# Optimization experiments

Hardware: AMD Instinct MI355X
Metric: run time of the kernel (lower is better)

The kernel has to match this reference:

```python
import jax, jax.numpy as jnp
import numpy as np

# ---- static config (mirrors PointRend init kwargs) ----
H, W = 512, 512          # img_size
CH, CW = 128, 128        # coarse_size
FH, FW = 256, 256        # fine_size
CF = 256                 # fine_channels
NC = 3                   # num_classes (forced by MLP's hard-coded 259/131 channel counts)
NPTS = 2048              # N points
K_OVER = 3               # k oversampling
BELTA = 0.75
NUM_OVER = K_OVER * NPTS          # 6144
STEP1 = int(NPTS * BELTA)         # 1536 uncertain points
STEP2 = NPTS - STEP1              # 512 coverage points


def _xavier(key, c_out, c_in):
    std = (2.0 / (c_in + c_out)) ** 0.5
    return jax.random.normal(key, (c_out, c_in), jnp.float32) * std


def setup_inputs() -> dict:
    key = jax.random.key(0)
    k1, k2, k3, k4, k5, k6 = jax.random.split(key, 6)
    fine_grained = jax.random.normal(k1, (2, CF, FH, FW), jnp.float32)
    coarse_pre = jax.random.normal(k2, (2, NC, CH, CW), jnp.float32)
    # torch.randperm(H*W) done inside forward in the original; passed in for determinism
    random_1d_index = jax.random.permutation(k3, H * W).astype(jnp.int32)
    w1 = _xavier(k4, 256, CF + NC)   # conv1: 1x1, in=259, out=256, no bias
    w2 = _xavier(k5, 128, 256 + 3)   # conv2: in=259, out=128
    w3 = _xavier(k6, NC, 128 + 3)    # conv3: in=131, out=num_classes
    prelu_a = jnp.array(0.25, jnp.float32)  # shared single-param PReLU
    return dict(fine_grained=fine_grained, coarse_pre=coarse_pre,
                w1=w1, w2=w2, w3=w3, prelu_a=prelu_a,
                random_1d_index=random_1d_index)


def _bilinear(x, h, w):
    # matches nn.Upsample(mode='bilinear', align_corners=False)
    return jax.image.resize(x, (x.shape[0], x.shape[1], h, w), method="bilinear")


def _prelu(x, a):
    return jnp.where(x >= 0, x, a * x)


def _mlp(feat, w1, w2, w3, a):
    # feat: [B, N, C] -> channels-first [B, C, N]; BatchNorms in MLP are unused in forward.
    x = jnp.transpose(feat, (0, 2, 1))
    tail = x[:, -3:, :]  # last 3 channels appended to each layer's input
    l1 = _prelu(jnp.einsum('bcn,oc->bon', x, w1), a)
    l2 = _prelu(jnp.einsum('bcn,oc->bon', jnp.concatenate([l1, tail], 1), w2), a)
    return jnp.einsum('bcn,oc->bon', jnp.concatenate([l2, tail], 1), w3)  # [B, NC, N]


def reference(fine_grained, coarse_pre, w1, w2, w3, prelu_a, random_1d_index):
    B = fine_grained.shape[0]
    up_coarse_o = _bilinear(coarse_pre, H, W)            # [B, NC, H, W] logits
    up_coarse_sm = jax.nn.softmax(up_coarse_o, axis=1)   # softmax over classes
    up_fine = _bilinear(fine_grained, H, W)              # [B, CF, H, W]

    h_idx = random_1d_index // W
    w_idx = random_1d_index % W
    all_index = jnp.stack([h_idx, w_idx], axis=1)        # [H*W, 2]
    cand = all_index[:NUM_OVER]                          # oversampled candidates

    # vectorized replacement of the python loop: gather probs at candidates
    over_pre = up_coarse_sm[:, :, cand[:, 0], cand[:, 1]].transpose(0, 2, 1)  # [B, NUM_OVER, NC]
    top2, _ = jax.lax.top_k(over_pre, 2)
    uncertain = 1.0 - (top2[..., 0] - top2[..., 1])      # [B, NUM_OVER]
    _, u_idx = jax.lax.top_k(uncertain, STEP1)           # [B, STEP1]
    u_pts = cand[u_idx]                                  # [B, STEP1, 2]
    cov = jnp.broadcast_to(all_index[-STEP2:][None], (B, STEP2, 2))
    pts = jnp.concatenate([u_pts, cov], axis=1)          # [B, N, 2]

    # masked_select traverses the dense mask in row-major (h,w) order -> sort linear ids
    lin = pts[..., 0] * W + pts[..., 1]                  # [B, N]
    lin_sorted = jnp.sort(lin, axis=1)
    sh, sw = lin_sorted // W, lin_sorted % W
    bidx = jnp.arange(B)[:, None]
    sel_coarse = up_coarse_o[bidx, :, sh, sw]            # [B, N, NC] (pre-softmax feats)
    sel_fine = up_fine[bidx, :, sh, sw]                  # [B, N, CF]

    # faithful to torch: flat concat of the two masked_select outputs, then reshape
    feat = jnp.concatenate([sel_fine.reshape(-1), sel_coarse.reshape(-1)]).reshape(B, NPTS, -1)

    out = _mlp(feat, w1, w2, w3, prelu_a)                # [B, NC, N]
    mask = jnp.zeros((B, H, W), jnp.int32).at[bidx, pts[..., 0], pts[..., 1]].add(1)
    return out, mask
```

## Files before the change

kernel.cpp:

```cpp
#include <hip/hip_runtime.h>
#include <hip/hip_bf16.h>

#define NPTS 2048
#define NOVER 6144
#define STEP1 1536
#define STEP2 512
#define HW_TOT 262144

__device__ __forceinline__ float prelu_f(float x, float a) { return x >= 0.0f ? x : a * x; }

__device__ __forceinline__ void coarse_coords(int h, int w, float& fy, float& fx,
                                              int& y0, int& y1, int& x0, int& x1) {
  float sy = (h + 0.5f) * 0.25f - 0.5f;
  float sx = (w + 0.5f) * 0.25f - 0.5f;
  float yf = floorf(sy), xf = floorf(sx);
  fy = sy - yf; fx = sx - xf;
  int yi = (int)yf, xi = (int)xf;
  y0 = min(127, max(0, yi)); y1 = min(127, max(0, yi + 1));
  x0 = min(127, max(0, xi)); x1 = min(127, max(0, xi + 1));
}

__device__ __forceinline__ float coarse_sample(const float* __restrict__ ch, float fy, float fx,
                                               int y0, int y1, int x0, int x1) {
  float v00 = ch[(y0 << 7) + x0];
  float v01 = ch[(y0 << 7) + x1];
  float v10 = ch[(y1 << 7) + x0];
  float v11 = ch[(y1 << 7) + x1];
  return (1.0f - fy) * ((1.0f - fx) * v00 + fx * v01) + fy * ((1.0f - fx) * v10 + fx * v11);
}

__global__ __launch_bounds__(256) void pr_fill_v4(uint4* __restrict__ p) {
  p[blockIdx.x * 256 + threadIdx.x] = make_uint4(0u, 0u, 0u, 0u);
}

__global__ __launch_bounds__(256) void pr_wprep_v4(const float* __restrict__ w1,
                                                   const float* __restrict__ w2,
                                                   float* __restrict__ wT1,
                                                   float* __restrict__ wT2) {
  int gid = blockIdx.x * 256 + threadIdx.x;
  if (gid < 259 * 256) {
    int c = gid >> 8, o = gid & 255;
    wT1[c * 256 + o] = w1[o * 259 + c];
  } else {
    int g2 = gid - 259 * 256;
    if (g2 < 259 * 128) {
      int c = g2 >> 7, o = g2 & 127;
      wT2[c * 128 + o] = w2[o * 259 + c];
    }
  }
}

__global__ __launch_bounds__(256) void pr_uncert_v4(const float* __restrict__ coarse,
                                                    const int* __restrict__ ridx,
                                                    unsigned* __restrict__ keys) {
  int gid = blockIdx.x * 256 + threadIdx.x;
  if (gid >= 2 * NOVER) return;
  int b = gid / NOVER, i = gid - b * NOVER;
  int lin = ridx[i];
  int h = lin >> 9, w = lin & 511;
  float fy, fx; int y0, y1, x0, x1;
  coarse_coords(h, w, fy, fx, y0, y1, x0, x1);
  const float* cb = coarse + (((size_t)b * 3) << 14);
  float p0 = coarse_sample(cb, fy, fx, y0, y1, x0, x1);
  float p1 = coarse_sample(cb + (1 << 14), fy, fx, y0, y1, x0, x1);
  float p2 = coarse_sample(cb + (2 << 14), fy, fx, y0, y1, x0, x1);
  float m = fmaxf(p0, fmaxf(p1, p2));
  float e0 = expf(p0 - m), e1 = expf(p1 - m), e2 = expf(p2 - m);
  float s = e0 + e1 + e2;
  float q0 = e0 / s, q1 = e1 / s, q2 = e2 / s;
  float a0 = q0, a1 = q1, a2 = q2, tmp;
  if (a0 < a1) { tmp = a0; a0 = a1; a1 = tmp; }
  if (a1 < a2) { tmp = a1; a1 = a2; a2 = tmp; }
  if (a0 < a1) { tmp = a0; a0 = a1; a1 = tmp; }
  float u = 1.0f - (a0 - a1);
  keys[gid] = __float_as_uint(u);
}

__global__ __launch_bounds__(1024) void pr_topk_v4(const unsigned* __restrict__ keys,
                                                   const int* __restrict__ ridx,
                                                   int* __restrict__ lin_sorted,
                                                   float* __restrict__ mask) {
  __shared__ unsigned kv[NOVER];
  __shared__ unsigned bitmap[8192];
  __shared__ unsigned hist[256];
  __shared__ unsigned short tiebuf[NOVER];
  __shared__ unsigned scanbuf[16];
  __shared__ unsigned selinfo[2];
  __shared__ int tiecnt;
  const int b = blockIdx.x, t = threadIdx.x;
  const int lane = t & 63, wid = t >> 6;

  for (int i = t; i < NOVER; i += 1024) kv[i] = keys[b * NOVER + i];
  for (int i = t; i < 8192; i += 1024) bitmap[i] = 0u;
  if (t == 0) { selinfo[1] = STEP1; tiecnt = 0; }
  __syncthreads();

  unsigned prefix = 0u;
  for (int pass = 0; pass < 4; ++pass) {
    const int shift = 24 - 8 * pass;
    const unsigned maskHi = (pass == 0) ? 0u : (0xFFFFFFFFu << (shift + 8));
    for (int i = t; i < 256; i += 1024) hist[i] = 0u;
    __syncthreads();
    for (int i = t; i < NOVER; i += 1024) {
      unsigned k = kv[i];
      if ((k & maskHi) == prefix) atomicAdd(&hist[(k >> shift) & 255u], 1u);
    }
    __syncthreads();
    if (t < 64) {
      unsigned h0 = hist[t * 4], h1 = hist[t * 4 + 1], h2 = hist[t * 4 + 2], h3 = hist[t * 4 + 3];
      unsigned q = h0 + h1 + h2 + h3;
      unsigned s = q;
      for (int off = 1; off < 64; off <<= 1) {
        unsigned n = __shfl_down(s, off);
        if (t + off < 64) s += n;
      }
      unsigned exq = s - q;
      unsigned R = selinfo[1];
      unsigned se3 = exq, se2 = se3 + h3, se1 = se2 + h2, se0 = se1 + h1;
      if (se3 < R && R <= se3 + h3)      { selinfo[0] = prefix | ((unsigned)(t * 4 + 3) << shift); selinfo[1] = R - se3; }
      else if (se2 < R && R <= se2 + h2) { selinfo[0] = prefix | ((unsigned)(t * 4 + 2) << shift); selinfo[1] = R - se2; }
      else if (se1 < R && R <= se1 + h1) { selinfo[0] = prefix | ((unsigned)(t * 4 + 1) << shift); selinfo[1] = R - se1; }
      else if (se0 < R && R <= se0 + h0) { selinfo[0] = prefix | ((unsigned)(t * 4 + 0) << shift); selinfo[1] = R - se0; }
    }
    __syncthreads();
    prefix = selinfo[0];
  }
  const unsigned T = prefix;
  const int r = (int)selinfo[1];

  for (int i = t; i < NOVER; i += 1024) {
    unsigned k = kv[i];
    if (k > T) {
      int lin = ridx[i];
      mask[(size_t)b * HW_TOT + lin] = 1.0f;
      atomicOr(&bitmap[lin >> 5], 1u << (lin & 31));
    } else if (k == T) {
      int pos = atomicAdd(&tiecnt, 1);
      tiebuf[pos] = (unsigned short)i;
    }
  }
  for (int i = t; i < STEP2; i += 1024) {
    int lin = ridx[HW_TOT - STEP2 + i];
    mask[(size_t)b * HW_TOT + lin] = 1.0f;
    atomicOr(&bitmap[lin >> 5], 1u << (lin & 31));
  }
  __syncthreads();
  const int m = tiecnt;
  for (int j = t; j < m; j += 1024) {
    int idx = tiebuf[j];
    int rank = 0;
    for (int jj = 0; jj < m; ++jj) rank += (tiebuf[jj] < idx) ? 1 : 0;
    if (rank < r) {
      int lin = ridx[idx];
      mask[(size_t)b * HW_TOT + lin] = 1.0f;
      atomicOr(&bitmap[lin >> 5], 1u << (lin & 31));
    }
  }
  __syncthreads();

  unsigned mySum = 0;
#pragma unroll
  for (int q = 0; q < 8; ++q) mySum += __popc(bitmap[t * 8 + q]);
  unsigned v = mySum;
  for (int off = 1; off < 64; off <<= 1) {
    unsigned n = __shfl_up(v, off);
    if (lane >= off) v += n;
  }
  if (lane == 63) scanbuf[wid] = v;
  __syncthreads();
  if (t == 0) {
    unsigned run = 0;
    for (int w16 = 0; w16 < 16; ++w16) { unsigned tmp = scanbuf[w16]; scanbuf[w16] = run; run += tmp; }
  }
  __syncthreads();
  unsigned pos = (v - mySum) + scanbuf[wid];
  for (int q = 0; q < 8; ++q) {
    unsigned word = bitmap[t * 8 + q];
    int basebit = (t * 8 + q) << 5;
    while (word) {
      int bit = __ffs(word) - 1;
      word &= word - 1;
      lin_sorted[b * NPTS + pos++] = basebit + bit;
    }
  }
}

__global__ __launch_bounds__(256) void pr_mlp_v4(const float* __restrict__ fine,
                                                 const float* __restrict__ coarse,
                                                 const float* __restrict__ wT1,
                                                 const float* __restrict__ wT2,
                                                 const float* __restrict__ w3,
                                                 const float* __restrict__ pa,
                                                 const int* __restrict__ lin_sorted,
                                                 float* __restrict__ out) {
  __shared__ __align__(16) float xs[259][16];
  __shared__ __align__(16) float l1t[256][16];
  __shared__ __align__(16) float l2t[128][16];
  const int t = threadIdx.x;
  const int g0 = blockIdx.x * 16;
  const float a = pa[0];

  for (int task = t; task < 259 * 16; task += 256) {
    int c = task >> 4, p = task & 15;
    int g = g0 + p;
    int j = g * 259 + c;
    float v;
    if (j < 1048576) {
      int nsrc = j >> 8, ch = j & 255;
      int bs = nsrc >> 11;
      int lin = lin_sorted[nsrc];
      int h = lin >> 9, w = lin & 511;
      float sy = (h + 0.5f) * 0.5f - 0.5f;
      float sx = (w + 0.5f) * 0.5f - 0.5f;
      float yf = floorf(sy), xf = floorf(sx);
      float fy = sy - yf, fx = sx - xf;
      int yi = (int)yf, xi = (int)xf;
      int y0 = min(255, max(0, yi)), y1 = min(255, max(0, yi + 1));
      int x0 = min(255, max(0, xi)), x1 = min(255, max(0, xi + 1));
      const float* base = fine + (((size_t)(bs * 256 + ch)) << 16);
      float v00 = base[(y0 << 8) + x0];
      float v01 = base[(y0 << 8) + x1];
      float v10 = base[(y1 << 8) + x0];
      float v11 = base[(y1 << 8) + x1];
      v = (1.0f - fy) * ((1.0f - fx) * v00 + fx * v01) + fy * ((1.0f - fx) * v10 + fx * v11);
    } else {
      int jj = j - 1048576;
      int nsrc = jj / 3;
      int kk = jj - nsrc * 3;
      int bs = nsrc >> 11;
      int lin = lin_sorted[nsrc];
      int h = lin >> 9, w = lin & 511;
      float fy, fx; int y0, y1, x0, x1;
      coarse_coords(h, w, fy, fx, y0, y1, x0, x1);
      v = coarse_sample(coarse + (((size_t)bs * 3 + kk) << 14), fy, fx, y0, y1, x0, x1);
    }
    xs[c][p] = v;
  }
  __syncthreads();

  {
    const int ob = (t & 63) * 4;
    const int pb = (t >> 6) * 4;
    float acc[4][4];
#pragma unroll
    for (int i = 0; i < 4; ++i)
#pragma unroll
      for (int q = 0; q < 4; ++q) acc[i][q] = 0.0f;
    for (int c = 0; c < 259; ++c) {
      const float4 wv = *(const float4*)&wT1[c * 256 + ob];
      const float4 xv = *(const float4*)&xs[c][pb];
      acc[0][0] = fmaf(wv.x, xv.x, acc[0][0]); acc[0][1] = fmaf(wv.x, xv.y, acc[0][1]);
      acc[0][2] = fmaf(wv.x, xv.z, acc[0][2]); acc[0][3] = fmaf(wv.x, xv.w, acc[0][3]);
      acc[1][0] = fmaf(wv.y, xv.x, acc[1][0]); acc[1][1] = fmaf(wv.y, xv.y, acc[1][1]);
      acc[1][2] = fmaf(wv.y, xv.z, acc[1][2]); acc[1][3] = fmaf(wv.y, xv.w, acc[1][3]);
      acc[2][0] = fmaf(wv.z, xv.x, acc[2][0]); acc[2][1] = fmaf(wv.z, xv.y, acc[2][1]);
      acc[2][2] = fmaf(wv.z, xv.z, acc[2][2]); acc[2][3] = fmaf(wv.z, xv.w, acc[2][3]);
      acc[3][0] = fmaf(wv.w, xv.x, acc[3][0]); acc[3][1] = fmaf(wv.w, xv.y, acc[3][1]);
      acc[3][2] = fmaf(wv.w, xv.z, acc[3][2]); acc[3][3] = fmaf(wv.w, xv.w, acc[3][3]);
    }
#pragma unroll
    for (int i = 0; i < 4; ++i) {
      l1t[ob + i][pb + 0] = prelu_f(acc[i][0], a);
      l1t[ob + i][pb + 1] = prelu_f(acc[i][1], a);
      l1t[ob + i][pb + 2] = prelu_f(acc[i][2], a);
      l1t[ob + i][pb + 3] = prelu_f(acc[i][3], a);
    }
  }
  __syncthreads();

  {
    const int ob = (t & 31) * 4;
    const int pb = (t >> 5) * 2;
    float acc[4][2];
#pragma unroll
    for (int i = 0; i < 4; ++i) { acc[i][0] = 0.0f; acc[i][1] = 0.0f; }
    for (int c = 0; c < 256; ++c) {
      const float4 wv = *(const float4*)&wT2[c * 128 + ob];
      const float2 xv = *(const float2*)&l1t[c][pb];
      acc[0][0] = fmaf(wv.x, xv.x, acc[0][0]); acc[0][1] = fmaf(wv.x, xv.y, acc[0][1]);
      acc[1][0] = fmaf(wv.y, xv.x, acc[1][0]); acc[1][1] = fmaf(wv.y, xv.y, acc[1][1]);
      acc[2][0] = fmaf(wv.z, xv.x, acc[2][0]); acc[2][1] = fmaf(wv.z, xv.y, acc[2][1]);
      acc[3][0] = fmaf(wv.w, xv.x, acc[3][0]); acc[3][1] = fmaf(wv.w, xv.y, acc[3][1]);
    }
#pragma unroll
    for (int kk = 0; kk < 3; ++kk) {
      const float4 wv = *(const float4*)&wT2[(256 + kk) * 128 + ob];
      const float x0 = xs[256 + kk][pb], x1 = xs[256 + kk][pb + 1];
      acc[0][0] = fmaf(wv.x, x0, acc[0][0]); acc[0][1] = fmaf(wv.x, x1, acc[0][1]);
      acc[1][0] = fmaf(wv.y, x0, acc[1][0]); acc[1][1] = fmaf(wv.y, x1, acc[1][1]);
      acc[2][0] = fmaf(wv.z, x0, acc[2][0]); acc[2][1] = fmaf(wv.z, x1, acc[2][1]);
      acc[3][0] = fmaf(wv.w, x0, acc[3][0]); acc[3][1] = fmaf(wv.w, x1, acc[3][1]);
    }
#pragma unroll
    for (int i = 0; i < 4; ++i) {
      l2t[ob + i][pb + 0] = prelu_f(acc[i][0], a);
      l2t[ob + i][pb + 1] = prelu_f(acc[i][1], a);
    }
  }
  __syncthreads();

  if (t < 48) {
    const int o3 = t % 3, p = t / 3;
    const float* wr = w3 + o3 * 131;
    float s = 0.0f;
    for (int c = 0; c < 128; ++c) s = fmaf(wr[c], l2t[c][p], s);
#pragma unroll
    for (int kk = 0; kk < 3; ++kk) s = fmaf(wr[128 + kk], xs[256 + kk][p], s);
    const int g = g0 + p;
    out[((g >> 11) * 3 + o3) * 2048 + (g & 2047)] = s;
  }
}

extern "C" void kernel_launch(void* const* d_in, const int* in_sizes, int n_in,
                              void* d_out, int out_size, void* d_ws, size_t ws_size,
                              hipStream_t stream) {
  const float* fine   = (const float*)d_in[0];
  const float* coarse = (const float*)d_in[1];
  const float* w1     = (const float*)d_in[2];
  const float* w2     = (const float*)d_in[3];
  const float* w3     = (const float*)d_in[4];
  const float* pa     = (const float*)d_in[5];
  const int*   ridx   = (const int*)d_in[6];

  float* out  = (float*)d_out;
  float* mask = out + 2 * 3 * 2048;

  char* ws = (char*)d_ws;
  int*      lin_sorted = (int*)ws;
  float*    wT1  = (float*)(ws + 16384);
  float*    wT2  = (float*)(ws + 16384 + 265216);
  unsigned* keys = (unsigned*)(ws + 16384 + 265216 + 132608);

  pr_fill_v4<<<512, 256, 0, stream>>>((uint4*)mask);
  pr_wprep_v4<<<389, 256, 0, stream>>>(w1, w2, wT1, wT2);
  pr_uncert_v4<<<48, 256, 0, stream>>>(coarse, ridx, keys);
  pr_topk_v4<<<2, 1024, 0, stream>>>(keys, ridx, lin_sorted, mask);
  pr_mlp_v4<<<256, 256, 0, stream>>>(fine, coarse, wT1, wT2, w3, pa, lin_sorted, out);
}
```

Baseline: 254.9 us.

## Fuse prep and uncertainty kernels, halve MLP tile to 8 points per block

Merges the mask fill and weight transpose into one launch, and computes the uncertainty keys directly inside the top-k kernel instead of in a separate kernel. This cuts the launch count from five to three and drops the keys round-trip through global memory. The MLP block now handles 8 points instead of 16, doubling the grid to 512 blocks for better CU coverage, and stores layer outputs point-major with float4 writes. The trade-off is less weight reuse per block, so each block rereads the transposed weights for fewer points, and the uncertainty work now runs on only 2 blocks.

Measured after the change: 313.5 us. +23.0%, slower.

```diff
diff --git a/kernel.cpp b/kernel.cpp
--- a/kernel.cpp
+++ b/kernel.cpp
@@ -1,5 +1,4 @@
 #include <hip/hip_runtime.h>
-#include <hip/hip_bf16.h>
 
 #define NPTS 2048
 #define NOVER 6144
@@ -29,15 +28,17 @@
   return (1.0f - fy) * ((1.0f - fx) * v00 + fx * v01) + fy * ((1.0f - fx) * v10 + fx * v11);
 }
 
-__global__ __launch_bounds__(256) void pr_fill_v4(uint4* __restrict__ p) {
-  p[blockIdx.x * 256 + threadIdx.x] = make_uint4(0u, 0u, 0u, 0u);
-}
-
-__global__ __launch_bounds__(256) void pr_wprep_v4(const float* __restrict__ w1,
-                                                   const float* __restrict__ w2,
-                                                   float* __restrict__ wT1,
-                                                   float* __restrict__ wT2) {
-  int gid = blockIdx.x * 256 + threadIdx.x;
+__global__ __launch_bounds__(256) void pr_prep_v5(uint4* __restrict__ mask4,
+                                                  const float* __restrict__ w1,
+                                                  const float* __restrict__ w2,
+                                                  float* __restrict__ wT1,
+                                                  float* __restrict__ wT2) {
+  const int bb = blockIdx.x;
+  if (bb < 512) {
+    mask4[bb * 256 + threadIdx.x] = make_uint4(0u, 0u, 0u, 0u);
+    return;
+  }
+  int gid = (bb - 512) * 256 + threadIdx.x;
   if (gid < 259 * 256) {
     int c = gid >> 8, o = gid & 255;
     wT1[c * 256 + o] = w1[o * 259 + c];
@@ -50,33 +51,7 @@
   }
 }
 
-__global__ __launch_bounds__(256) void pr_uncert_v4(const float* __restrict__ coarse,
-                                                    const int* __restrict__ ridx,
-                                                    unsigned* __restrict__ keys) {
-  int gid = blockIdx.x * 256 + threadIdx.x;
-  if (gid >= 2 * NOVER) return;
-  int b = gid / NOVER, i = gid - b * NOVER;
-  int lin = ridx[i];
-  int h = lin >> 9, w = lin & 511;
-  float fy, fx; int y0, y1, x0, x1;
-  coarse_coords(h, w, fy, fx, y0, y1, x0, x1);
-  const float* cb = coarse + (((size_t)b * 3) << 14);
-  float p0 = coarse_sample(cb, fy, fx, y0, y1, x0, x1);
-  float p1 = coarse_sample(cb + (1 << 14), fy, fx, y0, y1, x0, x1);
-  float p2 = coarse_sample(cb + (2 << 14), fy, fx, y0, y1, x0, x1);
-  float m = fmaxf(p0, fmaxf(p1, p2));
-  float e0 = expf(p0 - m), e1 = expf(p1 - m), e2 = expf(p2 - m);
-  float s = e0 + e1 + e2;
-  float q0 = e0 / s, q1 = e1 / s, q2 = e2 / s;
-  float a0 = q0, a1 = q1, a2 = q2, tmp;
-  if (a0 < a1) { tmp = a0; a0 = a1; a1 = tmp; }
-  if (a1 < a2) { tmp = a1; a1 = a2; a2 = tmp; }
-  if (a0 < a1) { tmp = a0; a0 = a1; a1 = tmp; }
-  float u = 1.0f - (a0 - a1);
-  keys[gid] = __float_as_uint(u);
-}
-
-__global__ __launch_bounds__(1024) void pr_topk_v4(const unsigned* __restrict__ keys,
+__global__ __launch_bounds__(1024) void pr_topk_v5(const float* __restrict__ coarse,
                                                    const int* __restrict__ ridx,
                                                    int* __restrict__ lin_sorted,
                                                    float* __restrict__ mask) {
@@ -90,7 +65,26 @@
   const int b = blockIdx.x, t = threadIdx.x;
   const int lane = t & 63, wid = t >> 6;
 
-  for (int i = t; i < NOVER; i += 1024) kv[i] = keys[b * NOVER + i];
+  const float* cb = coarse + (((size_t)b * 3) << 14);
+  for (int i = t; i < NOVER; i += 1024) {
+    int lin = ridx[i];
+    int h = lin >> 9, w = lin & 511;
+    float fy, fx; int y0, y1, x0, x1;
+    coarse_coords(h, w, fy, fx, y0, y1, x0, x1);
+    float p0 = coarse_sample(cb, fy, fx, y0, y1, x0, x1);
+    float p1 = coarse_sample(cb + (1 << 14), fy, fx, y0, y1, x0, x1);
+    float p2 = coarse_sample(cb + (2 << 14), fy, fx, y0, y1, x0, x1);
+    float m = fmaxf(p0, fmaxf(p1, p2));
+    float e0 = expf(p0 - m), e1 = expf(p1 - m), e2 = expf(p2 - m);
+    float s = e0 + e1 + e2;
+    float q0 = e0 / s, q1 = e1 / s, q2 = e2 / s;
+    float a0 = q0, a1 = q1, a2 = q2, tmp;
+    if (a0 < a1) { tmp = a0; a0 = a1; a1 = tmp; }
+    if (a1 < a2) { tmp = a1; a1 = a2; a2 = tmp; }
+    if (a0 < a1) { tmp = a0; a0 = a1; a1 = tmp; }
+    float u = 1.0f - (a0 - a1);
+    kv[i] = __float_as_uint(u);
+  }
   for (int i = t; i < 8192; i += 1024) bitmap[i] = 0u;
   if (t == 0) { selinfo[1] = STEP1; tiecnt = 0; }
   __syncthreads();
@@ -185,7 +179,7 @@
   }
 }
 
-__global__ __launch_bounds__(256) void pr_mlp_v4(const float* __restrict__ fine,
+__global__ __launch_bounds__(256) void pr_mlp_v5(const float* __restrict__ fine,
                                                  const float* __restrict__ coarse,
                                                  const float* __restrict__ wT1,
                                                  const float* __restrict__ wT2,
@@ -193,15 +187,15 @@
                                                  const float* __restrict__ pa,
                                                  const int* __restrict__ lin_sorted,
                                                  float* __restrict__ out) {
-  __shared__ __align__(16) float xs[259][16];
-  __shared__ __align__(16) float l1t[256][16];
-  __shared__ __align__(16) float l2t[128][16];
+  __shared__ __align__(16) float xs[259][8];
+  __shared__ __align__(16) float l1p[8][260];
+  __shared__ __align__(16) float l2p[8][132];
   const int t = threadIdx.x;
-  const int g0 = blockIdx.x * 16;
+  const int g0 = blockIdx.x * 8;
   const float a = pa[0];
 
-  for (int task = t; task < 259 * 16; task += 256) {
-    int c = task >> 4, p = task & 15;
+  for (int task = t; task < 259 * 8; task += 256) {
+    int c = task >> 3, p = task & 7;
     int g = g0 + p;
     int j = g * 259 + c;
     float v;
@@ -240,70 +234,73 @@
 
   {
     const int ob = (t & 63) * 4;
-    const int pb = (t >> 6) * 4;
-    float acc[4][4];
-#pragma unroll
-    for (int i = 0; i < 4; ++i)
-#pragma unroll
-      for (int q = 0; q < 4; ++q) acc[i][q] = 0.0f;
+    const int pq = (t >> 6) * 2;
+    float acc[4][2];
+#pragma unroll
+    for (int i = 0; i < 4; ++i) { acc[i][0] = 0.0f; acc[i][1] = 0.0f; }
+#pragma unroll 4
     for (int c = 0; c < 259; ++c) {
       const float4 wv = *(const float4*)&wT1[c * 256 + ob];
-      const float4 xv = *(const float4*)&xs[c][pb];
-      acc[0][0] = fmaf(wv.x, xv.x, acc[0][0]); acc[0][1] = fmaf(wv.x, xv.y, acc[0][1]);
-      acc[0][2] = fmaf(wv.x, xv.z, acc[0][2]); acc[0][3] = fmaf(wv.x, xv.w, acc[0][3]);
-      acc[1][0] = fmaf(wv.y, xv.x, acc[1][0]); acc[1][1] = fmaf(wv.y, xv.y, acc[1][1]);
-      acc[1][2] = fmaf(wv.y, xv.z, acc[1][2]); acc[1][3] = fmaf(wv.y, xv.w, acc[1][3]);
-      acc[2][0] = fmaf(wv.z, xv.x, acc[2][0]); acc[2][1] = fmaf(wv.z, xv.y, acc[2][1]);
-      acc[2][2] = fmaf(wv.z, xv.z, acc[2][2]); acc[2][3] = fmaf(wv.z, xv.w, acc[2][3]);
-      acc[3][0] = fmaf(wv.w, xv.x, acc[3][0]); acc[3][1] = fmaf(wv.w, xv.y, acc[3][1]);
-      acc[3][2] = fmaf(wv.w, xv.z, acc[3][2]); acc[3][3] = fmaf(wv.w, xv.w, acc[3][3]);
-    }
-#pragma unroll
-    for (int i = 0; i < 4; ++i) {
-      l1t[ob + i][pb + 0] = prelu_f(acc[i][0], a);
-      l1t[ob + i][pb + 1] = prelu_f(acc[i][1], a);
-      l1t[ob + i][pb + 2] = prelu_f(acc[i][2], a);
-      l1t[ob + i][pb + 3] = prelu_f(acc[i][3], a);
-    }
-  }
-  __syncthreads();
-
-  {
-    const int ob = (t & 31) * 4;
-    const int pb = (t >> 5) * 2;
-    float acc[4][2];
-#pragma unroll
-    for (int i = 0; i < 4; ++i) { acc[i][0] = 0.0f; acc[i][1] = 0.0f; }
-    for (int c = 0; c < 256; ++c) {
-      const float4 wv = *(const float4*)&wT2[c * 128 + ob];
-      const float2 xv = *(const float2*)&l1t[c][pb];
+      const float2 xv = *(const float2*)&xs[c][pq];
       acc[0][0] = fmaf(wv.x, xv.x, acc[0][0]); acc[0][1] = fmaf(wv.x, xv.y, acc[0][1]);
       acc[1][0] = fmaf(wv.y, xv.x, acc[1][0]); acc[1][1] = fmaf(wv.y, xv.y, acc[1][1]);
       acc[2][0] = fmaf(wv.z, xv.x, acc[2][0]); acc[2][1] = fmaf(wv.z, xv.y, acc[2][1]);
       acc[3][0] = fmaf(wv.w, xv.x, acc[3][0]); acc[3][1] = fmaf(wv.w, xv.y, acc[3][1]);
     }
 #pragma unroll
+    for (int q = 0; q < 2; ++q) {
+      float4 o;
+      o.x = prelu_f(acc[0][q], a);
+      o.y = prelu_f(acc[1][q], a);
+      o.z = prelu_f(acc[2][q], a);
+      o.w = prelu_f(acc[3][q], a);
+      *(float4*)&l1p[pq + q][ob] = o;
+    }
+  }
+  __syncthreads();
+
+  {
+    const int ob = (t & 31) * 4;
+    const int pt = (t >> 5);
+    float acc[4] = {0.0f, 0.0f, 0.0f, 0.0f};
+#pragma unroll 4
+    for (int c = 0; c < 256; c += 4) {
+      const float4 xv = *(const float4*)&l1p[pt][c];
+      const float4 w0 = *(const float4*)&wT2[(c + 0) * 128 + ob];
+      const float4 w1 = *(const float4*)&wT2[(c + 1) * 128 + ob];
+      const float4 w2 = *(const float4*)&wT2[(c + 2) * 128 + ob];
+      const float4 w3v = *(const float4*)&wT2[(c + 3) * 128 + ob];
+      acc[0] = fmaf(w0.x, xv.x, acc[0]); acc[1] = fmaf(w0.y, xv.x, acc[1]);
+      acc[2] = fmaf(w0.z, xv.x, acc[2]); acc[3] = fmaf(w0.w, xv.x, acc[3]);
+      acc[0] = fmaf(w1.x, xv.y, acc[0]); acc[1] = fmaf(w1.y, xv.y, acc[1]);
+      acc[2] = fmaf(w1.z, xv.y, acc[2]); acc[3] = fmaf(w1.w, xv.y, acc[3]);
+      acc[0] = fmaf(w2.x, xv.z, acc[0]); acc[1] = fmaf(w2.y, xv.z, acc[1]);
+      acc[2] = fmaf(w2.z, xv.z, acc[2]); acc[3] = fmaf(w2.w, xv.z, acc[3]);
+      acc[0] = fmaf(w3v.x, xv.w, acc[0]); acc[1] = fmaf(w3v.y, xv.w, acc[1]);
+      acc[2] = fmaf(w3v.z, xv.w, acc[2]); acc[3] = fmaf(w3v.w, xv.w, acc[3]);
+    }
+#pragma unroll
     for (int kk = 0; kk < 3; ++kk) {
       const float4 wv = *(const float4*)&wT2[(256 + kk) * 128 + ob];
-      const float x0 = xs[256 + kk][pb], x1 = xs[256 + kk][pb + 1];
-      acc[0][0] = fmaf(wv.x, x0, acc[0][0]); acc[0][1] = fmaf(wv.x, x1, acc[0][1]);
-      acc[1][0] = fmaf(wv.y, x0, acc[1][0]); acc[1][1] = fmaf(wv.y, x1, acc[1][1]);
-      acc[2][0] = fmaf(wv.z, x0, acc[2][0]); acc[2][1] = fmaf(wv.z, x1, acc[2][1]);
-      acc[3][0] = fmaf(wv.w, x0, acc[3][0]); acc[3][1] = fmaf(wv.w, x1, acc[3][1]);
-    }
-#pragma unroll
-    for (int i = 0; i < 4; ++i) {
-      l2t[ob + i][pb + 0] = prelu_f(acc[i][0], a);
-      l2t[ob + i][pb + 1] = prelu_f(acc[i][1], a);
-    }
-  }
-  __syncthreads();
-
-  if (t < 48) {
+      const float x0 = xs[256 + kk][pt];
+      acc[0] = fmaf(wv.x, x0, acc[0]); acc[1] = fmaf(wv.y, x0, acc[1]);
+      acc[2] = fmaf(wv.z, x0, acc[2]); acc[3] = fmaf(wv.w, x0, acc[3]);
+    }
+    float4 o;
+    o.x = prelu_f(acc[0], a);
+    o.y = prelu_f(acc[1], a);
+    o.z = prelu_f(acc[2], a);
+    o.w = prelu_f(acc[3], a);
+    *(float4*)&l2p[pt][ob] = o;
+  }
+  __syncthreads();
+
+  if (t < 24) {
     const int o3 = t % 3, p = t / 3;
     const float* wr = w3 + o3 * 131;
     float s = 0.0f;
-    for (int c = 0; c < 128; ++c) s = fmaf(wr[c], l2t[c][p], s);
+#pragma unroll 4
+    for (int c = 0; c < 128; ++c) s = fmaf(wr[c], l2p[p][c], s);
 #pragma unroll
     for (int kk = 0; kk < 3; ++kk) s = fmaf(wr[128 + kk], xs[256 + kk][p], s);
     const int g = g0 + p;
@@ -326,14 +323,11 @@
   float* mask = out + 2 * 3 * 2048;
 
   char* ws = (char*)d_ws;
-  int*      lin_sorted = (int*)ws;
-  float*    wT1  = (float*)(ws + 16384);
-  float*    wT2  = (float*)(ws + 16384 + 265216);
-  unsigned* keys = (unsigned*)(ws + 16384 + 265216 + 132608);
-
-  pr_fill_v4<<<512, 256, 0, stream>>>((uint4*)mask);
-  pr_wprep_v4<<<389, 256, 0, stream>>>(w1, w2, wT1, wT2);
-  pr_uncert_v4<<<48, 256, 0, stream>>>(coarse, ridx, keys);
-  pr_topk_v4<<<2, 1024, 0, stream>>>(keys, ridx, lin_sorted, mask);
-  pr_mlp_v4<<<256, 256, 0, stream>>>(fine, coarse, wT1, wT2, w3, pa, lin_sorted, out);
-}
+  int*   lin_sorted = (int*)ws;
+  float* wT1  = (float*)(ws + 16384);
+  float* wT2  = (float*)(ws + 16384 + 265216);
+
+  pr_prep_v5<<<901, 256, 0, stream>>>((uint4*)mask, w1, w2, wT1, wT2);
+  pr_topk_v5<<<2, 1024, 0, stream>>>(coarse, ridx, lin_sorted, mask);
+  pr_mlp_v5<<<512, 256, 0, stream>>>(fine, coarse, wT1, wT2, w3, pa, lin_sorted, out);
+}
```

## Stage MLP weights through double-buffered LDS tiles with 512-thread blocks

Applied to the files above, without the earlier changes.

The MLP kernel now streams the transposed layer-1 and layer-2 weights through a double-buffered shared-memory tile, issuing the register prefetch of the next 32KB chunk while the current chunk is consumed. Blocks grow to 512 threads, with per-thread work reduced to a 4x2 tile for layer 1 and 4 outputs for layer 2. Intermediate activations switch to a point-major layout. The goal is to replace repeated global/L2 weight reads with LDS reads and hide load latency, at the cost of about 100KB LDS per block (limiting occupancy) and a barrier per chunk.

Measured after the change: 274.1 us. 1.08x slower.

```diff
diff --git a/kernel.cpp b/kernel.cpp
--- a/kernel.cpp
+++ b/kernel.cpp
@@ -1,5 +1,4 @@
 #include <hip/hip_runtime.h>
-#include <hip/hip_bf16.h>
 
 #define NPTS 2048
 #define NOVER 6144
@@ -185,7 +184,7 @@
   }
 }
 
-__global__ __launch_bounds__(256) void pr_mlp_v4(const float* __restrict__ fine,
+__global__ __launch_bounds__(512) void pr_mlp_v6(const float* __restrict__ fine,
                                                  const float* __restrict__ coarse,
                                                  const float* __restrict__ wT1,
                                                  const float* __restrict__ wT2,
@@ -193,14 +192,30 @@
                                                  const float* __restrict__ pa,
                                                  const int* __restrict__ lin_sorted,
                                                  float* __restrict__ out) {
+  __shared__ __align__(16) float wbuf[2][8192];
   __shared__ __align__(16) float xs[259][16];
-  __shared__ __align__(16) float l1t[256][16];
-  __shared__ __align__(16) float l2t[128][16];
+  __shared__ __align__(16) float l1p[16][260];
+  __shared__ __align__(16) float l2p[16][132];
   const int t = threadIdx.x;
   const int g0 = blockIdx.x * 16;
   const float a = pa[0];
 
-  for (int task = t; task < 259 * 16; task += 256) {
+  const int ob1 = (t & 63) * 4;
+  const int pq1 = (t >> 6) * 2;
+  const int ob2 = (t & 31) * 4;
+  const int pt2 = t >> 5;
+
+  float4 t1[3], t2[3];
+#pragma unroll
+  for (int i = 0; i < 3; ++i) {
+    t1[i] = *(const float4*)&wT1[(256 + i) * 256 + ob1];
+    t2[i] = *(const float4*)&wT2[(256 + i) * 128 + ob2];
+  }
+  float4 st[4];
+#pragma unroll
+  for (int j = 0; j < 4; ++j) st[j] = *(const float4*)&wT1[(j * 512 + t) * 4];
+
+  for (int task = t; task < 259 * 16; task += 512) {
     int c = task >> 4, p = task & 15;
     int g = g0 + p;
     int j = g * 259 + c;
@@ -236,74 +251,105 @@
     }
     xs[c][p] = v;
   }
-  __syncthreads();
-
-  {
-    const int ob = (t & 63) * 4;
-    const int pb = (t >> 6) * 4;
-    float acc[4][4];
-#pragma unroll
-    for (int i = 0; i < 4; ++i)
-#pragma unroll
-      for (int q = 0; q < 4; ++q) acc[i][q] = 0.0f;
-    for (int c = 0; c < 259; ++c) {
-      const float4 wv = *(const float4*)&wT1[c * 256 + ob];
-      const float4 xv = *(const float4*)&xs[c][pb];
-      acc[0][0] = fmaf(wv.x, xv.x, acc[0][0]); acc[0][1] = fmaf(wv.x, xv.y, acc[0][1]);
-      acc[0][2] = fmaf(wv.x, xv.z, acc[0][2]); acc[0][3] = fmaf(wv.x, xv.w, acc[0][3]);
-      acc[1][0] = fmaf(wv.y, xv.x, acc[1][0]); acc[1][1] = fmaf(wv.y, xv.y, acc[1][1]);
-      acc[1][2] = fmaf(wv.y, xv.z, acc[1][2]); acc[1][3] = fmaf(wv.y, xv.w, acc[1][3]);
-      acc[2][0] = fmaf(wv.z, xv.x, acc[2][0]); acc[2][1] = fmaf(wv.z, xv.y, acc[2][1]);
-      acc[2][2] = fmaf(wv.z, xv.z, acc[2][2]); acc[2][3] = fmaf(wv.z, xv.w, acc[2][3]);
-      acc[3][0] = fmaf(wv.w, xv.x, acc[3][0]); acc[3][1] = fmaf(wv.w, xv.y, acc[3][1]);
-      acc[3][2] = fmaf(wv.w, xv.z, acc[3][2]); acc[3][3] = fmaf(wv.w, xv.w, acc[3][3]);
-    }
-#pragma unroll
-    for (int i = 0; i < 4; ++i) {
-      l1t[ob + i][pb + 0] = prelu_f(acc[i][0], a);
-      l1t[ob + i][pb + 1] = prelu_f(acc[i][1], a);
-      l1t[ob + i][pb + 2] = prelu_f(acc[i][2], a);
-      l1t[ob + i][pb + 3] = prelu_f(acc[i][3], a);
-    }
-  }
-  __syncthreads();
-
-  {
-    const int ob = (t & 31) * 4;
-    const int pb = (t >> 5) * 2;
-    float acc[4][2];
-#pragma unroll
-    for (int i = 0; i < 4; ++i) { acc[i][0] = 0.0f; acc[i][1] = 0.0f; }
-    for (int c = 0; c < 256; ++c) {
-      const float4 wv = *(const float4*)&wT2[c * 128 + ob];
-      const float2 xv = *(const float2*)&l1t[c][pb];
-      acc[0][0] = fmaf(wv.x, xv.x, acc[0][0]); acc[0][1] = fmaf(wv.x, xv.y, acc[0][1]);
-      acc[1][0] = fmaf(wv.y, xv.x, acc[1][0]); acc[1][1] = fmaf(wv.y, xv.y, acc[1][1]);
-      acc[2][0] = fmaf(wv.z, xv.x, acc[2][0]); acc[2][1] = fmaf(wv.z, xv.y, acc[2][1]);
-      acc[3][0] = fmaf(wv.w, xv.x, acc[3][0]); acc[3][1] = fmaf(wv.w, xv.y, acc[3][1]);
-    }
-#pragma unroll
-    for (int kk = 0; kk < 3; ++kk) {
-      const float4 wv = *(const float4*)&wT2[(256 + kk) * 128 + ob];
-      const float x0 = xs[256 + kk][pb], x1 = xs[256 + kk][pb + 1];
-      acc[0][0] = fmaf(wv.x, x0, acc[0][0]); acc[0][1] = fmaf(wv.x, x1, acc[0][1]);
-      acc[1][0] = fmaf(wv.y, x0, acc[1][0]); acc[1][1] = fmaf(wv.y, x1, acc[1][1]);
-      acc[2][0] = fmaf(wv.z, x0, acc[2][0]); acc[2][1] = fmaf(wv.z, x1, acc[2][1]);
-      acc[3][0] = fmaf(wv.w, x0, acc[3][0]); acc[3][1] = fmaf(wv.w, x1, acc[3][1]);
-    }
-#pragma unroll
-    for (int i = 0; i < 4; ++i) {
-      l2t[ob + i][pb + 0] = prelu_f(acc[i][0], a);
-      l2t[ob + i][pb + 1] = prelu_f(acc[i][1], a);
-    }
-  }
-  __syncthreads();
+#pragma unroll
+  for (int j = 0; j < 4; ++j) *(float4*)&wbuf[0][(j * 512 + t) * 4] = st[j];
+  __syncthreads();
+
+  float acc1[4][2];
+#pragma unroll
+  for (int i = 0; i < 4; ++i) { acc1[i][0] = 0.0f; acc1[i][1] = 0.0f; }
+  float acc2[4] = {0.0f, 0.0f, 0.0f, 0.0f};
+
+  for (int k = 0; k < 12; ++k) {
+    const int cur = k & 1;
+    if (k < 11) {
+      const float* src;
+      if (k < 7)       src = wT1 + (k + 1) * 8192;
+      else if (k == 7) src = wT2;
+      else             src = wT2 + (k - 7) * 8192;
+#pragma unroll
+      for (int j = 0; j < 4; ++j) st[j] = *(const float4*)&src[(j * 512 + t) * 4];
+    }
+
+    if (k < 8) {
+      const float* w = wbuf[cur];
+      const int c0 = k * 32;
+#pragma unroll 8
+      for (int cl = 0; cl < 32; ++cl) {
+        const float4 wv = *(const float4*)&w[cl * 256 + ob1];
+        const float2 xv = *(const float2*)&xs[c0 + cl][pq1];
+        acc1[0][0] = fmaf(wv.x, xv.x, acc1[0][0]); acc1[0][1] = fmaf(wv.x, xv.y, acc1[0][1]);
+        acc1[1][0] = fmaf(wv.y, xv.x, acc1[1][0]); acc1[1][1] = fmaf(wv.y, xv.y, acc1[1][1]);
+        acc1[2][0] = fmaf(wv.z, xv.x, acc1[2][0]); acc1[2][1] = fmaf(wv.z, xv.y, acc1[2][1]);
+        acc1[3][0] = fmaf(wv.w, xv.x, acc1[3][0]); acc1[3][1] = fmaf(wv.w, xv.y, acc1[3][1]);
+      }
+      if (k == 7) {
+#pragma unroll
+        for (int i = 0; i < 3; ++i) {
+          const float2 xv = *(const float2*)&xs[256 + i][pq1];
+          acc1[0][0] = fmaf(t1[i].x, xv.x, acc1[0][0]); acc1[0][1] = fmaf(t1[i].x, xv.y, acc1[0][1]);
+          acc1[1][0] = fmaf(t1[i].y, xv.x, acc1[1][0]); acc1[1][1] = fmaf(t1[i].y, xv.y, acc1[1][1]);
+          acc1[2][0] = fmaf(t1[i].z, xv.x, acc1[2][0]); acc1[2][1] = fmaf(t1[i].z, xv.y, acc1[2][1]);
+          acc1[3][0] = fmaf(t1[i].w, xv.x, acc1[3][0]); acc1[3][1] = fmaf(t1[i].w, xv.y, acc1[3][1]);
+        }
+#pragma unroll
+        for (int q = 0; q < 2; ++q) {
+          float4 o;
+          o.x = prelu_f(acc1[0][q], a);
+          o.y = prelu_f(acc1[1][q], a);
+          o.z = prelu_f(acc1[2][q], a);
+          o.w = prelu_f(acc1[3][q], a);
+          *(float4*)&l1p[pq1 + q][ob1] = o;
+        }
+      }
+    } else {
+      const float* w = wbuf[cur];
+      const int c0 = (k - 8) * 64;
+#pragma unroll 4
+      for (int cl = 0; cl < 64; cl += 4) {
+        const float4 xv = *(const float4*)&l1p[pt2][c0 + cl];
+        const float4 w0 = *(const float4*)&w[(cl + 0) * 128 + ob2];
+        const float4 w1v = *(const float4*)&w[(cl + 1) * 128 + ob2];
+        const float4 w2v = *(const float4*)&w[(cl + 2) * 128 + ob2];
+        const float4 w3v = *(const float4*)&w[(cl + 3) * 128 + ob2];
+        acc2[0] = fmaf(w0.x, xv.x, acc2[0]); acc2[1] = fmaf(w0.y, xv.x, acc2[1]);
+        acc2[2] = fmaf(w0.z, xv.x, acc2[2]); acc2[3] = fmaf(w0.w, xv.x, acc2[3]);
+        acc2[0] = fmaf(w1v.x, xv.y, acc2[0]); acc2[1] = fmaf(w1v.y, xv.y, acc2[1]);
+        acc2[2] = fmaf(w1v.z, xv.y, acc2[2]); acc2[3] = fmaf(w1v.w, xv.y, acc2[3]);
+        acc2[0] = fmaf(w2v.x, xv.z, acc2[0]); acc2[1] = fmaf(w2v.y, xv.z, acc2[1]);
+        acc2[2] = fmaf(w2v.z, xv.z, acc2[2]); acc2[3] = fmaf(w2v.w, xv.z, acc2[3]);
+        acc2[0] = fmaf(w3v.x, xv.w, acc2[0]); acc2[1] = fmaf(w3v.y, xv.w, acc2[1]);
+        acc2[2] = fmaf(w3v.z, xv.w, acc2[2]); acc2[3] = fmaf(w3v.w, xv.w, acc2[3]);
+      }
+      if (k == 11) {
+#pragma unroll
+        for (int i = 0; i < 3; ++i) {
+          const float x0 = xs[256 + i][pt2];
+          acc2[0] = fmaf(t2[i].x, x0, acc2[0]); acc2[1] = fmaf(t2[i].y, x0, acc2[1]);
+          acc2[2] = fmaf(t2[i].z, x0, acc2[2]); acc2[3] = fmaf(t2[i].w, x0, acc2[3]);
+        }
+        float4 o;
+        o.x = prelu_f(acc2[0], a);
+        o.y = prelu_f(acc2[1], a);
+        o.z = prelu_f(acc2[2], a);
+        o.w = prelu_f(acc2[3], a);
+        *(float4*)&l2p[pt2][ob2] = o;
+      }
+    }
+
+    if (k < 11) {
+#pragma unroll
+      for (int j = 0; j < 4; ++j) *(float4*)&wbuf[cur ^ 1][(j * 512 + t) * 4] = st[j];
+    }
+    __syncthreads();
+  }
 
   if (t < 48) {
     const int o3 = t % 3, p = t / 3;
     const float* wr = w3 + o3 * 131;
     float s = 0.0f;
-    for (int c = 0; c < 128; ++c) s = fmaf(wr[c], l2t[c][p], s);
+#pragma unroll 4
+    for (int c = 0; c < 128; ++c) s = fmaf(wr[c], l2p[p][c], s);
 #pragma unroll
     for (int kk = 0; kk < 3; ++kk) s = fmaf(wr[128 + kk], xs[256 + kk][p], s);
     const int g = g0 + p;
@@ -335,5 +381,5 @@
   pr_wprep_v4<<<389, 256, 0, stream>>>(w1, w2, wT1, wT2);
   pr_uncert_v4<<<48, 256, 0, stream>>>(coarse, ridx, keys);
   pr_topk_v4<<<2, 1024, 0, stream>>>(keys, ridx, lin_sorted, mask);
-  pr_mlp_v4<<<256, 256, 0, stream>>>(fine, coarse, wT1, wT2, w3, pa, lin_sorted, out);
-}
+  pr_mlp_v6<<<256, 512, 0, stream>>>(fine, coarse, wT1, wT2, w3, pa, lin_sorted, out);
+}
```

## Split bilinear gather into separate kernel and shrink MLP blocks to 8 points

Applied to the files above, without the earlier changes.

Moves the bilinear sampling of fine and coarse features out of the MLP kernel into a dedicated gather kernel. That kernel writes channel-major intermediate buffers in the workspace, so the irregular per-element index math and scattered reads run in a fully parallel launch instead of serialising inside each MLP block. The MLP kernel then processes 8 points per 128-thread block, doubling the block count for more parallelism, and adds partial loop unrolling. The cost is an extra kernel launch and a round trip through global memory of about 4 MB of intermediates. Each MLP block also re-reads the full weight matrices for fewer points.

After: 338.6 us. +32.8%, slower.

```diff
diff --git a/kernel.cpp b/kernel.cpp
--- a/kernel.cpp
+++ b/kernel.cpp
@@ -1,5 +1,4 @@
 #include <hip/hip_runtime.h>
-#include <hip/hip_bf16.h>
 
 #define NPTS 2048
 #define NOVER 6144
@@ -185,54 +184,66 @@
   }
 }
 
-__global__ __launch_bounds__(256) void pr_mlp_v4(const float* __restrict__ fine,
-                                                 const float* __restrict__ coarse,
-                                                 const float* __restrict__ wT1,
-                                                 const float* __restrict__ wT2,
-                                                 const float* __restrict__ w3,
-                                                 const float* __restrict__ pa,
-                                                 const int* __restrict__ lin_sorted,
-                                                 float* __restrict__ out) {
-  __shared__ __align__(16) float xs[259][16];
-  __shared__ __align__(16) float l1t[256][16];
-  __shared__ __align__(16) float l2t[128][16];
+__global__ __launch_bounds__(256) void pr_gather_v7(const float* __restrict__ fine,
+                                                    const float* __restrict__ coarse,
+                                                    const int* __restrict__ lin_sorted,
+                                                    float* __restrict__ fineval,
+                                                    float* __restrict__ cval) {
+  const int tid = blockIdx.x * 256 + threadIdx.x;
+  if (tid < 1048576) {
+    const int s = tid & 4095, ch = tid >> 12;
+    const int bs = s >> 11;
+    const int lin = lin_sorted[s];
+    const int h = lin >> 9, w = lin & 511;
+    float sy = (h + 0.5f) * 0.5f - 0.5f;
+    float sx = (w + 0.5f) * 0.5f - 0.5f;
+    float yf = floorf(sy), xf = floorf(sx);
+    float fy = sy - yf, fx = sx - xf;
+    int yi = (int)yf, xi = (int)xf;
+    int y0 = min(255, max(0, yi)), y1 = min(255, max(0, yi + 1));
+    int x0 = min(255, max(0, xi)), x1 = min(255, max(0, xi + 1));
+    const float* base = fine + (((size_t)(bs * 256 + ch)) << 16);
+    float v00 = base[(y0 << 8) + x0];
+    float v01 = base[(y0 << 8) + x1];
+    float v10 = base[(y1 << 8) + x0];
+    float v11 = base[(y1 << 8) + x1];
+    fineval[tid] = (1.0f - fy) * ((1.0f - fx) * v00 + fx * v01)
+                 + fy * ((1.0f - fx) * v10 + fx * v11);
+  } else {
+    const int u = tid - 1048576;
+    const int s = u & 4095, kk = u >> 12;
+    const int bs = s >> 11;
+    const int lin = lin_sorted[s];
+    const int h = lin >> 9, w = lin & 511;
+    float fy, fx; int y0, y1, x0, x1;
+    coarse_coords(h, w, fy, fx, y0, y1, x0, x1);
+    cval[u] = coarse_sample(coarse + (((size_t)bs * 3 + kk) << 14), fy, fx, y0, y1, x0, x1);
+  }
+}
+
+__global__ __launch_bounds__(128) void pr_mlpc_v7(const float* __restrict__ fineval,
+                                                  const float* __restrict__ cval,
+                                                  const float* __restrict__ wT1,
+                                                  const float* __restrict__ wT2,
+                                                  const float* __restrict__ w3,
+                                                  const float* __restrict__ pa,
+                                                  float* __restrict__ out) {
+  __shared__ __align__(16) float xs[259][8];
+  __shared__ __align__(16) float l1t[256][8];
+  __shared__ __align__(16) float l2t[128][8];
   const int t = threadIdx.x;
-  const int g0 = blockIdx.x * 16;
+  const int g0 = blockIdx.x * 8;
   const float a = pa[0];
 
-  for (int task = t; task < 259 * 16; task += 256) {
-    int c = task >> 4, p = task & 15;
-    int g = g0 + p;
-    int j = g * 259 + c;
+  for (int task = t; task < 259 * 8; task += 128) {
+    int c = task >> 3, p = task & 7;
+    int j = (g0 + p) * 259 + c;
     float v;
     if (j < 1048576) {
-      int nsrc = j >> 8, ch = j & 255;
-      int bs = nsrc >> 11;
-      int lin = lin_sorted[nsrc];
-      int h = lin >> 9, w = lin & 511;
-      float sy = (h + 0.5f) * 0.5f - 0.5f;
-      float sx = (w + 0.5f) * 0.5f - 0.5f;
-      float yf = floorf(sy), xf = floorf(sx);
-      float fy = sy - yf, fx = sx - xf;
-      int yi = (int)yf, xi = (int)xf;
-      int y0 = min(255, max(0, yi)), y1 = min(255, max(0, yi + 1));
-      int x0 = min(255, max(0, xi)), x1 = min(255, max(0, xi + 1));
-      const float* base = fine + (((size_t)(bs * 256 + ch)) << 16);
-      float v00 = base[(y0 << 8) + x0];
-      float v01 = base[(y0 << 8) + x1];
-      float v10 = base[(y1 << 8) + x0];
-      float v11 = base[(y1 << 8) + x1];
-      v = (1.0f - fy) * ((1.0f - fx) * v00 + fx * v01) + fy * ((1.0f - fx) * v10 + fx * v11);
+      v = fineval[(j & 255) * 4096 + (j >> 8)];
     } else {
       int jj = j - 1048576;
-      int nsrc = jj / 3;
-      int kk = jj - nsrc * 3;
-      int bs = nsrc >> 11;
-      int lin = lin_sorted[nsrc];
-      int h = lin >> 9, w = lin & 511;
-      float fy, fx; int y0, y1, x0, x1;
-      coarse_coords(h, w, fy, fx, y0, y1, x0, x1);
-      v = coarse_sample(coarse + (((size_t)bs * 3 + kk) << 14), fy, fx, y0, y1, x0, x1);
+      v = cval[(jj % 3) * 4096 + jj / 3];
     }
     xs[c][p] = v;
   }
@@ -246,6 +257,7 @@
     for (int i = 0; i < 4; ++i)
 #pragma unroll
       for (int q = 0; q < 4; ++q) acc[i][q] = 0.0f;
+#pragma unroll 2
     for (int c = 0; c < 259; ++c) {
       const float4 wv = *(const float4*)&wT1[c * 256 + ob];
       const float4 xv = *(const float4*)&xs[c][pb];
@@ -274,6 +286,7 @@
     float acc[4][2];
 #pragma unroll
     for (int i = 0; i < 4; ++i) { acc[i][0] = 0.0f; acc[i][1] = 0.0f; }
+#pragma unroll 2
     for (int c = 0; c < 256; ++c) {
       const float4 wv = *(const float4*)&wT2[c * 128 + ob];
       const float2 xv = *(const float2*)&l1t[c][pb];
@@ -299,10 +312,11 @@
   }
   __syncthreads();
 
-  if (t < 48) {
+  if (t < 24) {
     const int o3 = t % 3, p = t / 3;
     const float* wr = w3 + o3 * 131;
     float s = 0.0f;
+#pragma unroll 4
     for (int c = 0; c < 128; ++c) s = fmaf(wr[c], l2t[c][p], s);
 #pragma unroll
     for (int kk = 0; kk < 3; ++kk) s = fmaf(wr[128 + kk], xs[256 + kk][p], s);
@@ -327,13 +341,16 @@
 
   char* ws = (char*)d_ws;
   int*      lin_sorted = (int*)ws;
-  float*    wT1  = (float*)(ws + 16384);
-  float*    wT2  = (float*)(ws + 16384 + 265216);
-  unsigned* keys = (unsigned*)(ws + 16384 + 265216 + 132608);
+  float*    wT1     = (float*)(ws + 16384);
+  float*    wT2     = (float*)(ws + 281600);
+  unsigned* keys    = (unsigned*)(ws + 414208);
+  float*    fineval = (float*)(ws + 463360);
+  float*    cval    = (float*)(ws + 4657664);
 
   pr_fill_v4<<<512, 256, 0, stream>>>((uint4*)mask);
   pr_wprep_v4<<<389, 256, 0, stream>>>(w1, w2, wT1, wT2);
   pr_uncert_v4<<<48, 256, 0, stream>>>(coarse, ridx, keys);
   pr_topk_v4<<<2, 1024, 0, stream>>>(keys, ridx, lin_sorted, mask);
-  pr_mlp_v4<<<256, 256, 0, stream>>>(fine, coarse, wT1, wT2, w3, pa, lin_sorted, out);
-}
+  pr_gather_v7<<<4144, 256, 0, stream>>>(fine, coarse, lin_sorted, fineval, cval);
+  pr_mlpc_v7<<<512, 128, 0, stream>>>(fineval, cval, wT1, wT2, w3, pa, out);
+}
```
